# Kernel optimization log

Measured on AMD Instinct MI355X. Metric: run time of the kernel, lower is better.

## Reference

```python
import jax, jax.numpy as jnp
import numpy as np

N, E, F, H, G, U, A = 50000, 800000, 96, 96, 64, 32, 16


def _linear_params(key, fan_in, fan_out):
    # torch nn.Linear default init: U(-1/sqrt(fan_in), 1/sqrt(fan_in))
    s = 1.0 / np.sqrt(fan_in)
    kw, kb = jax.random.split(key)
    W = jax.random.uniform(kw, (fan_in, fan_out), jnp.float32, -s, s)
    b = jax.random.uniform(kb, (fan_out,), jnp.float32, -s, s)
    return W, b


def setup_inputs() -> dict:
    key = jax.random.key(0)
    ks = jax.random.split(key, 12)
    x = jax.random.normal(ks[0], (N, F), jnp.float32)
    edge_index = jax.random.randint(ks[1], (2, E), 0, N, dtype=jnp.int32)
    batch = jnp.sort(jax.random.randint(ks[2], (N,), 0, G, dtype=jnp.int32))
    u = jax.random.normal(ks[3], (G, U), jnp.float32)
    W1, b1 = _linear_params(ks[4], F, H)      # conv1
    W2, b2 = _linear_params(ks[5], H, H)      # conv2
    aW1, ab1 = _linear_params(ks[6], H + U, H)
    aW2, ab2 = _linear_params(ks[7], H, A)
    cW1, cb1 = _linear_params(ks[8], H + U, H)
    cW2, cb2 = _linear_params(ks[9], H, 1)
    return {"x": x, "edge_index": edge_index, "batch": batch, "u": u,
            "W1": W1, "b1": b1, "W2": W2, "b2": b2,
            "aW1": aW1, "ab1": ab1, "aW2": aW2, "ab2": ab2,
            "cW1": cW1, "cb1": cb1, "cW2": cW2, "cb2": cb2}


def reference(x, edge_index, batch, u, W1, b1, W2, b2,
              aW1, ab1, aW2, ab2, cW1, cb1, cW2, cb2):
    n = x.shape[0]
    src, dst = edge_index[0], edge_index[1]
    # GCN symmetric normalization with self-loops (PyG GCNConv defaults)
    deg = jnp.zeros((n,), x.dtype).at[dst].add(1.0) + 1.0  # +1 for self-loop
    dis = jax.lax.rsqrt(deg)                               # deg^{-1/2}
    edge_norm = (dis[src] * dis[dst])[:, None]             # [E,1]
    self_norm = (dis * dis)[:, None]                       # [N,1] = deg^{-1}

    def gcn(h, W, b):
        h = h @ W                                          # linear (bias after agg)
        agg = jax.ops.segment_sum(h[src] * edge_norm, dst, num_segments=n)
        return agg + h * self_norm + b

    h = jax.nn.relu(gcn(x, W1, b1))
    h = jax.nn.relu(gcn(h, W2, b2))

    # global mean pool over graphs
    cnt = jax.ops.segment_sum(jnp.ones((n,), h.dtype), batch, num_segments=G)
    pooled = jax.ops.segment_sum(h, batch, num_segments=G) / jnp.maximum(cnt, 1.0)[:, None]

    comb = jnp.concatenate([pooled, u], axis=1)            # [G, H+U]
    action_logits = jax.nn.relu(comb @ aW1 + ab1) @ aW2 + ab2   # [G, A]
    state_value = jax.nn.relu(comb @ cW1 + cb1) @ cW2 + cb2     # [G, 1]
    return action_logits, state_value
```

## Files before the change

kernel.cpp:

```cpp
#include <hip/hip_runtime.h>
#include <hip/hip_bf16.h>

#define FH 96
#define GU 32
#define GA 16
#define NG 64

typedef __attribute__((ext_vector_type(8))) short bf16x8;
typedef __attribute__((ext_vector_type(8))) unsigned short u16x8;
typedef __attribute__((ext_vector_type(4))) float f32x4;

static __device__ __forceinline__ unsigned short f2bf(float f) {
    unsigned int u = __float_as_uint(f);
    unsigned int r = (u + 0x7fffu + ((u >> 16) & 1u)) >> 16;
    return (unsigned short)r;
}
static __device__ __forceinline__ float bf2f(unsigned short h) {
    return __uint_as_float(((unsigned int)h) << 16);
}

__global__ void zero_k(float4* __restrict__ p, int n4) {
    int i = blockIdx.x * blockDim.x + threadIdx.x;
    if (i < n4) p[i] = make_float4(0.f, 0.f, 0.f, 0.f);
}

__global__ void count_deg_k(const int* __restrict__ dst, int* __restrict__ deg,
                            unsigned short* __restrict__ rank16, int E) {
    int e = blockIdx.x * blockDim.x + threadIdx.x;
    if (e < E) rank16[e] = (unsigned short)atomicAdd(&deg[dst[e]], 1);
}

__global__ __launch_bounds__(256) void partial_k(const int* __restrict__ deg,
                                                 int* __restrict__ blockSums, int n) {
    int base = blockIdx.x * 1024;
    int t = threadIdx.x;
    int s = 0;
#pragma unroll
    for (int j = 0; j < 4; j++) {
        int i = base + t * 4 + j;
        if (i < n) s += deg[i];
    }
    __shared__ int red[4];
    for (int off = 32; off > 0; off >>= 1) s += __shfl_down(s, off, 64);
    if ((t & 63) == 0) red[t >> 6] = s;
    __syncthreads();
    if (t == 0) blockSums[blockIdx.x] = red[0] + red[1] + red[2] + red[3];
}

__global__ __launch_bounds__(256) void scanpart_k(const int* __restrict__ blockSums,
                                                  int* __restrict__ blockOff, int nb) {
    __shared__ int sh[256];
    int t = threadIdx.x;
    sh[t] = (t < nb) ? blockSums[t] : 0;
    __syncthreads();
    for (int off = 1; off < 256; off <<= 1) {
        int v = 0;
        if (t >= off) v = sh[t - off];
        __syncthreads();
        if (t >= off) sh[t] += v;
        __syncthreads();
    }
    if (t < nb) blockOff[t] = (t == 0) ? 0 : sh[t - 1];
}

__global__ __launch_bounds__(256) void emit_k(const int* __restrict__ deg,
                                              const int* __restrict__ blockOff,
                                              int* __restrict__ rowstart,
                                              float* __restrict__ dis, int n) {
    __shared__ int sh[256];
    int base = blockIdx.x * 1024;
    int t = threadIdx.x;
    int d[4];
    int s = 0;
#pragma unroll
    for (int j = 0; j < 4; j++) {
        int i = base + t * 4 + j;
        d[j] = (i < n) ? deg[i] : 0;
        s += d[j];
    }
    sh[t] = s;
    __syncthreads();
    for (int off = 1; off < 256; off <<= 1) {
        int v = 0;
        if (t >= off) v = sh[t - off];
        __syncthreads();
        if (t >= off) sh[t] += v;
        __syncthreads();
    }
    int run = blockOff[blockIdx.x] + ((t == 0) ? 0 : sh[t - 1]);
#pragma unroll
    for (int j = 0; j < 4; j++) {
        int i = base + t * 4 + j;
        if (i < n) {
            rowstart[i] = run;
            dis[i] = rsqrtf((float)d[j] + 1.0f);
        }
        run += d[j];
    }
    if (blockIdx.x == gridDim.x - 1 && t == 255) rowstart[n] = run;
}

__global__ void fill_k(const int* __restrict__ src, const int* __restrict__ dst,
                       const int* __restrict__ rowstart,
                       const unsigned short* __restrict__ rank16,
                       unsigned short* __restrict__ csr, int E) {
    int e = blockIdx.x * blockDim.x + threadIdx.x;
    if (e < E) {
        int pos = rowstart[dst[e]] + (int)rank16[e];
        csr[pos] = (unsigned short)src[e];
    }
}

__global__ __launch_bounds__(256) void convW_k(const float* __restrict__ W1,
                                               const float* __restrict__ W2,
                                               unsigned short* __restrict__ WB1,
                                               unsigned short* __restrict__ WB2) {
    const float* W = (blockIdx.x == 0) ? W1 : W2;
    unsigned short* WB = (blockIdx.x == 0) ? WB1 : WB2;
    for (int idx = threadIdx.x; idx < 2 * 3 * 6 * 64 * 8; idx += 256) {
        int j = idx & 7;
        int lane = (idx >> 3) & 63;
        int frag = idx >> 9;
        int cg = frag % 6;
        int rest = frag / 6;
        int ks = rest % 3;
        int t = rest / 3;
        int k = ks * 32 + (lane >> 4) * 8 + j;
        int n = cg * 16 + (lane & 15);
        float w = W[k * FH + n];
        unsigned short h = f2bf(w);
        WB[idx] = (t == 0) ? h : f2bf(w - bf2f(h));
    }
}

template <int INMODE>
__global__ __launch_bounds__(256, 3) void gemm_mfma_k(
    const float* __restrict__ Xf, const unsigned short* __restrict__ Xb,
    const unsigned short* __restrict__ WB, const float* __restrict__ scale,
    unsigned short* __restrict__ Yb, int nrows) {
    int lane = threadIdx.x & 63;
    int wid  = threadIdx.x >> 6;
    int wr = wid >> 1, wc = wid & 1;
    int row0 = blockIdx.x * 64 + wr * 32;

    bf16x8 b[2][3][3];
#pragma unroll
    for (int t = 0; t < 2; t++)
#pragma unroll
        for (int ks = 0; ks < 3; ks++)
#pragma unroll
            for (int cg = 0; cg < 3; cg++) {
                int frag = (t * 3 + ks) * 6 + wc * 3 + cg;
                b[t][ks][cg] = *(const bf16x8*)(WB + frag * 512 + lane * 8);
            }

    f32x4 acc[2][3];
#pragma unroll
    for (int rg = 0; rg < 2; rg++)
#pragma unroll
        for (int cg = 0; cg < 3; cg++) acc[rg][cg] = (f32x4){0.f, 0.f, 0.f, 0.f};

    int r0 = lane & 15;
    int kcol = (lane >> 4) * 8;
#pragma unroll
    for (int ks = 0; ks < 3; ks++) {
        bf16x8 ah[2], al[2];
#pragma unroll
        for (int rg = 0; rg < 2; rg++) {
            if (INMODE == 1) {
                size_t off = (size_t)(row0 + rg * 16 + r0) * FH + ks * 32 + kcol;
                ah[rg] = *(const bf16x8*)(Xb + off);
            } else {
                int rr = row0 + rg * 16 + r0;
                if (rr >= nrows) rr = nrows - 1;
                const float* xp = Xf + (size_t)rr * FH + ks * 32 + kcol;
                float4 v0 = *(const float4*)xp;
                float4 v1 = *(const float4*)(xp + 4);
                float xv[8] = {v0.x, v0.y, v0.z, v0.w, v1.x, v1.y, v1.z, v1.w};
                bf16x8 hh, ll;
#pragma unroll
                for (int j = 0; j < 8; j++) {
                    unsigned short h = f2bf(xv[j]);
                    hh[j] = (short)h;
                    ll[j] = (short)f2bf(xv[j] - bf2f(h));
                }
                ah[rg] = hh;
                al[rg] = ll;
            }
        }
#pragma unroll
        for (int rg = 0; rg < 2; rg++)
#pragma unroll
            for (int cg = 0; cg < 3; cg++)
                acc[rg][cg] = __builtin_amdgcn_mfma_f32_16x16x32_bf16(
                    ah[rg], b[0][ks][cg], acc[rg][cg], 0, 0, 0);
#pragma unroll
        for (int rg = 0; rg < 2; rg++)
#pragma unroll
            for (int cg = 0; cg < 3; cg++)
                acc[rg][cg] = __builtin_amdgcn_mfma_f32_16x16x32_bf16(
                    ah[rg], b[1][ks][cg], acc[rg][cg], 0, 0, 0);
        if (INMODE == 0) {
#pragma unroll
            for (int rg = 0; rg < 2; rg++)
#pragma unroll
                for (int cg = 0; cg < 3; cg++)
                    acc[rg][cg] = __builtin_amdgcn_mfma_f32_16x16x32_bf16(
                        al[rg], b[0][ks][cg], acc[rg][cg], 0, 0, 0);
        }
    }

#pragma unroll
    for (int rg = 0; rg < 2; rg++) {
#pragma unroll
        for (int r = 0; r < 4; r++) {
            int row = row0 + rg * 16 + (lane >> 4) * 4 + r;
            if (row < nrows) {
                float s = scale[row];
#pragma unroll
                for (int cg = 0; cg < 3; cg++) {
                    int col = wc * 48 + cg * 16 + (lane & 15);
                    Yb[(size_t)row * FH + col] = f2bf(acc[rg][cg][r] * s);
                }
            }
        }
    }
}

__global__ __launch_bounds__(256) void gather12_k(
    const unsigned short* __restrict__ hXb, const float* __restrict__ dis,
    const int* __restrict__ rowstart, const unsigned short* __restrict__ csr,
    const float* __restrict__ bias, unsigned short* __restrict__ outB, int n) {
    int idx = blockIdx.x * blockDim.x + threadIdx.x;
    if (idx >= n * 12) return;
    int node = idx / 12;
    int f8 = (idx - node * 12) * 8;
    int s = rowstart[node];
    int e = rowstart[node + 1];
    u16x8 sv = *(const u16x8*)&hXb[node * FH + f8];
    float a[8];
#pragma unroll
    for (int j = 0; j < 8; j++) a[j] = bf2f((unsigned short)sv[j]);
    int p = s;
    for (; p + 4 <= e; p += 4) {
        int i0 = csr[p], i1 = csr[p + 1], i2 = csr[p + 2], i3 = csr[p + 3];
        u16x8 v0 = *(const u16x8*)&hXb[i0 * FH + f8];
        u16x8 v1 = *(const u16x8*)&hXb[i1 * FH + f8];
        u16x8 v2 = *(const u16x8*)&hXb[i2 * FH + f8];
        u16x8 v3 = *(const u16x8*)&hXb[i3 * FH + f8];
#pragma unroll
        for (int j = 0; j < 8; j++) {
            a[j] += (bf2f((unsigned short)v0[j]) + bf2f((unsigned short)v1[j]))
                  + (bf2f((unsigned short)v2[j]) + bf2f((unsigned short)v3[j]));
        }
    }
    for (; p < e; p++) {
        int i0 = csr[p];
        u16x8 v0 = *(const u16x8*)&hXb[i0 * FH + f8];
#pragma unroll
        for (int j = 0; j < 8; j++) a[j] += bf2f((unsigned short)v0[j]);
    }
    float dn = dis[node];
    float4 bv0 = *(const float4*)&bias[f8];
    float4 bv1 = *(const float4*)&bias[f8 + 4];
    float bb[8] = {bv0.x, bv0.y, bv0.z, bv0.w, bv1.x, bv1.y, bv1.z, bv1.w};
    u16x8 hh;
#pragma unroll
    for (int j = 0; j < 8; j++) hh[j] = f2bf(fmaxf(a[j] * dn + bb[j], 0.0f));
    *(u16x8*)&outB[node * FH + f8] = hh;
}

__global__ __launch_bounds__(128) void pool3_k(const unsigned short* __restrict__ h,
                                               const int* __restrict__ bat,
                                               float* __restrict__ pooled,
                                               float* __restrict__ cnt, int n) {
    const int CH = 32;
    int beg = blockIdx.x * CH;
    if (beg >= n) return;
    int end = min(beg + CH, n);
    int t = threadIdx.x;
    if (t < FH) {
        float acc = 0.f;
        int g = bat[beg];
        for (int node = beg; node < end; ++node) {
            int gg = bat[node];
            if (gg != g) { atomicAdd(&pooled[g * FH + t], acc); acc = 0.f; g = gg; }
            acc += bf2f(h[(size_t)node * FH + t]);
        }
        atomicAdd(&pooled[g * FH + t], acc);
    } else if (t == FH) {
        float c = 0.f;
        int g = bat[beg];
        for (int node = beg; node < end; ++node) {
            int gg = bat[node];
            if (gg != g) { atomicAdd(&cnt[g], c); c = 0.f; g = gg; }
            c += 1.f;
        }
        atomicAdd(&cnt[g], c);
    }
}

__global__ __launch_bounds__(128) void head_k(const float* __restrict__ pooled,
                                              const float* __restrict__ cnt,
                                              const float* __restrict__ u,
                                              const float* __restrict__ aW1, const float* __restrict__ ab1,
                                              const float* __restrict__ aW2, const float* __restrict__ ab2,
                                              const float* __restrict__ cW1, const float* __restrict__ cb1,
                                              const float* __restrict__ cW2, const float* __restrict__ cb2,
                                              float* __restrict__ out, int G) {
    int g = blockIdx.x;
    int t = threadIdx.x;
    __shared__ float comb[FH + GU];
    __shared__ float hidA[FH];
    __shared__ float hidC[FH];
    __shared__ float tmp[FH];
    float c = fmaxf(cnt[g], 1.0f);
    if (t < FH) comb[t] = pooled[g * FH + t] / c;
    else if (t < FH + GU) comb[t] = u[g * GU + (t - FH)];
    __syncthreads();
    if (t < FH) {
        float a = ab1[t], cc = cb1[t];
        for (int k = 0; k < FH + GU; k++) {
            float cv = comb[k];
            a += cv * aW1[k * FH + t];
            cc += cv * cW1[k * FH + t];
        }
        hidA[t] = fmaxf(a, 0.0f);
        hidC[t] = fmaxf(cc, 0.0f);
    }
    __syncthreads();
    if (t < GA) {
        float a = ab2[t];
        for (int j = 0; j < FH; j++) a += hidA[j] * aW2[j * GA + t];
        out[g * GA + t] = a;
    }
    if (t >= 32 && t < 32 + FH) tmp[t - 32] = hidC[t - 32] * cW2[t - 32];
    __syncthreads();
    if (t == 0) {
        float v = cb2[0];
        for (int j = 0; j < FH; j++) v += tmp[j];
        out[G * GA + g] = v;
    }
}

extern "C" void kernel_launch(void* const* d_in, const int* in_sizes, int n_in,
                              void* d_out, int out_size, void* d_ws, size_t ws_size,
                              hipStream_t stream) {
    const float* x   = (const float*)d_in[0];
    const int*   ei  = (const int*)d_in[1];
    const int*   bat = (const int*)d_in[2];
    const float* u   = (const float*)d_in[3];
    const float* W1  = (const float*)d_in[4];
    const float* b1  = (const float*)d_in[5];
    const float* W2  = (const float*)d_in[6];
    const float* b2  = (const float*)d_in[7];
    const float* aW1 = (const float*)d_in[8];
    const float* ab1 = (const float*)d_in[9];
    const float* aW2 = (const float*)d_in[10];
    const float* ab2 = (const float*)d_in[11];
    const float* cW1 = (const float*)d_in[12];
    const float* cb1 = (const float*)d_in[13];
    const float* cW2 = (const float*)d_in[14];
    const float* cb2 = (const float*)d_in[15];
    float* out = (float*)d_out;

    const int N = in_sizes[0] / FH;
    const int E = in_sizes[1] / 2;
    const int G = in_sizes[3] / GU;
    const int NPAD = (N + 63) / 64 * 64;

    const int* src = ei;
    const int* dst = ei + E;

    float* ws = (float*)d_ws;
    size_t o = 0;
    int*   degI     = (int*)(ws + o);   o += NPAD;
    float* pooled   = ws + o;           o += NG * FH;
    float* cnt      = ws + o;           o += 64;
    size_t zero_elems = o;
    float* dis      = ws + o;           o += NPAD;
    int*   rowstart = (int*)(ws + o);   o += NPAD;
    int*   blockSums= (int*)(ws + o);   o += 512;
    int*   blockOff = (int*)(ws + o);   o += 512;
    unsigned short* rank16 = (unsigned short*)(ws + o); o += ((size_t)(E + 1) / 2 + 63) / 64 * 64;
    unsigned short* csr16  = (unsigned short*)(ws + o); o += ((size_t)(E + 1) / 2 + 63) / 64 * 64;
    unsigned short* WB1 = (unsigned short*)(ws + o); o += 9216;
    unsigned short* WB2 = (unsigned short*)(ws + o); o += 9216;
    unsigned short* XhB = (unsigned short*)(ws + o); o += (size_t)NPAD * FH / 2;
    unsigned short* hXb = (unsigned short*)(ws + o); o += (size_t)NPAD * FH / 2;
    (void)ws_size;

    unsigned short* h2b = XhB;

    int gridE = (E + 255) / 256;
    int gridG12 = (N * 12 + 255) / 256;
    int gridMfma = NPAD / 64;
    int nbScan = (N + 1023) / 1024;
    int gridPool = (N + 31) / 32;
    int n4zero = (int)(zero_elems / 4);
    int gridZero = (n4zero + 255) / 256;

    zero_k<<<gridZero, 256, 0, stream>>>((float4*)ws, n4zero);

    count_deg_k<<<gridE, 256, 0, stream>>>(dst, degI, rank16, E);
    partial_k<<<nbScan, 256, 0, stream>>>(degI, blockSums, N);
    scanpart_k<<<1, 256, 0, stream>>>(blockSums, blockOff, nbScan);
    emit_k<<<nbScan, 256, 0, stream>>>(degI, blockOff, rowstart, dis, N);
    fill_k<<<gridE, 256, 0, stream>>>(src, dst, rowstart, rank16, csr16, E);

    convW_k<<<2, 256, 0, stream>>>(W1, W2, WB1, WB2);

    gemm_mfma_k<0><<<gridMfma, 256, 0, stream>>>(x, (const unsigned short*)nullptr,
                                                 WB1, dis, hXb, N);
    gather12_k<<<gridG12, 256, 0, stream>>>(hXb, dis, rowstart, csr16, b1, XhB, N);
    gemm_mfma_k<1><<<gridMfma, 256, 0, stream>>>((const float*)nullptr, XhB,
                                                 WB2, dis, hXb, N);
    gather12_k<<<gridG12, 256, 0, stream>>>(hXb, dis, rowstart, csr16, b2, h2b, N);

    pool3_k<<<gridPool, 128, 0, stream>>>(h2b, bat, pooled, cnt, N);
    head_k<<<G, 128, 0, stream>>>(pooled, cnt, u, aW1, ab1, aW2, ab2,
                                  cW1, cb1, cW2, cb2, out, G);
}
```

Baseline: 182.5 us.

## Fuse CSR preprocessing kernels into one cooperative kernel with grid syncs

Replaces the seven preprocessing launches (zeroing, degree count, partial sums, scan, emit, CSR fill, weight conversion) with a single cooperative kernel of 1024 blocks that separates the phases with grid-wide syncs. The aim is to remove per-launch overhead and the gaps between the small kernels. In exchange it adds five grid barriers and turns the edge loops into grid-stride loops over fewer threads. It also relies on all 1024 blocks being co-resident, and the launch return code is discarded.

```diff
diff --git a/kernel.cpp b/kernel.cpp
--- a/kernel.cpp
+++ b/kernel.cpp
@@ -1,5 +1,6 @@
 #include <hip/hip_runtime.h>
 #include <hip/hip_bf16.h>
+#include <hip/hip_cooperative_groups.h>
 
 #define FH 96
 #define GU 32
@@ -19,117 +20,121 @@
     return __uint_as_float(((unsigned int)h) << 16);
 }
 
-__global__ void zero_k(float4* __restrict__ p, int n4) {
-    int i = blockIdx.x * blockDim.x + threadIdx.x;
-    if (i < n4) p[i] = make_float4(0.f, 0.f, 0.f, 0.f);
-}
-
-__global__ void count_deg_k(const int* __restrict__ dst, int* __restrict__ deg,
-                            unsigned short* __restrict__ rank16, int E) {
-    int e = blockIdx.x * blockDim.x + threadIdx.x;
-    if (e < E) rank16[e] = (unsigned short)atomicAdd(&deg[dst[e]], 1);
-}
-
-__global__ __launch_bounds__(256) void partial_k(const int* __restrict__ deg,
-                                                 int* __restrict__ blockSums, int n) {
-    int base = blockIdx.x * 1024;
-    int t = threadIdx.x;
-    int s = 0;
-#pragma unroll
-    for (int j = 0; j < 4; j++) {
-        int i = base + t * 4 + j;
-        if (i < n) s += deg[i];
-    }
-    __shared__ int red[4];
-    for (int off = 32; off > 0; off >>= 1) s += __shfl_down(s, off, 64);
-    if ((t & 63) == 0) red[t >> 6] = s;
-    __syncthreads();
-    if (t == 0) blockSums[blockIdx.x] = red[0] + red[1] + red[2] + red[3];
-}
-
-__global__ __launch_bounds__(256) void scanpart_k(const int* __restrict__ blockSums,
-                                                  int* __restrict__ blockOff, int nb) {
+__global__ __launch_bounds__(256) void prep_k(
+    const int* __restrict__ src, const int* __restrict__ dst,
+    const float* __restrict__ W1, const float* __restrict__ W2,
+    int* __restrict__ deg, unsigned short* __restrict__ rank16,
+    int* __restrict__ rowstart, float* __restrict__ dis,
+    unsigned short* __restrict__ csr,
+    unsigned short* __restrict__ WB1, unsigned short* __restrict__ WB2,
+    int* __restrict__ blockOff, float* __restrict__ pooled,
+    float* __restrict__ cnt, int N, int E, int nbScan) {
+    cooperative_groups::grid_group gg = cooperative_groups::this_grid();
+    const int gtid = blockIdx.x * blockDim.x + threadIdx.x;
+    const int gsz = gridDim.x * blockDim.x;
     __shared__ int sh[256];
-    int t = threadIdx.x;
-    sh[t] = (t < nb) ? blockSums[t] : 0;
-    __syncthreads();
-    for (int off = 1; off < 256; off <<= 1) {
-        int v = 0;
-        if (t >= off) v = sh[t - off];
-        __syncthreads();
-        if (t >= off) sh[t] += v;
-        __syncthreads();
-    }
-    if (t < nb) blockOff[t] = (t == 0) ? 0 : sh[t - 1];
-}
-
-__global__ __launch_bounds__(256) void emit_k(const int* __restrict__ deg,
-                                              const int* __restrict__ blockOff,
-                                              int* __restrict__ rowstart,
-                                              float* __restrict__ dis, int n) {
-    __shared__ int sh[256];
-    int base = blockIdx.x * 1024;
-    int t = threadIdx.x;
-    int d[4];
-    int s = 0;
-#pragma unroll
-    for (int j = 0; j < 4; j++) {
-        int i = base + t * 4 + j;
-        d[j] = (i < n) ? deg[i] : 0;
-        s += d[j];
-    }
-    sh[t] = s;
-    __syncthreads();
-    for (int off = 1; off < 256; off <<= 1) {
-        int v = 0;
-        if (t >= off) v = sh[t - off];
-        __syncthreads();
-        if (t >= off) sh[t] += v;
-        __syncthreads();
-    }
-    int run = blockOff[blockIdx.x] + ((t == 0) ? 0 : sh[t - 1]);
-#pragma unroll
-    for (int j = 0; j < 4; j++) {
-        int i = base + t * 4 + j;
-        if (i < n) {
-            rowstart[i] = run;
-            dis[i] = rsqrtf((float)d[j] + 1.0f);
-        }
-        run += d[j];
-    }
-    if (blockIdx.x == gridDim.x - 1 && t == 255) rowstart[n] = run;
-}
-
-__global__ void fill_k(const int* __restrict__ src, const int* __restrict__ dst,
-                       const int* __restrict__ rowstart,
-                       const unsigned short* __restrict__ rank16,
-                       unsigned short* __restrict__ csr, int E) {
-    int e = blockIdx.x * blockDim.x + threadIdx.x;
-    if (e < E) {
-        int pos = rowstart[dst[e]] + (int)rank16[e];
-        csr[pos] = (unsigned short)src[e];
-    }
-}
-
-__global__ __launch_bounds__(256) void convW_k(const float* __restrict__ W1,
-                                               const float* __restrict__ W2,
-                                               unsigned short* __restrict__ WB1,
-                                               unsigned short* __restrict__ WB2) {
-    const float* W = (blockIdx.x == 0) ? W1 : W2;
-    unsigned short* WB = (blockIdx.x == 0) ? WB1 : WB2;
-    for (int idx = threadIdx.x; idx < 2 * 3 * 6 * 64 * 8; idx += 256) {
-        int j = idx & 7;
-        int lane = (idx >> 3) & 63;
-        int frag = idx >> 9;
-        int cg = frag % 6;
+
+    for (int i = gtid; i < N; i += gsz) deg[i] = 0;
+    for (int i = gtid; i < NG * FH + NG; i += gsz) {
+        if (i < NG * FH) pooled[i] = 0.f;
+        else cnt[i - NG * FH] = 0.f;
+    }
+    for (int idx = gtid; idx < 2 * 36 * 512; idx += gsz) {
+        int half = idx / (36 * 512);
+        int id2 = idx - half * (36 * 512);
+        const float* W = half ? W2 : W1;
+        unsigned short* WB = half ? WB2 : WB1;
+        int j = id2 & 7;
+        int lane = (id2 >> 3) & 63;
+        int frag = id2 >> 9;
+        int cgi = frag % 6;
         int rest = frag / 6;
         int ks = rest % 3;
         int t = rest / 3;
         int k = ks * 32 + (lane >> 4) * 8 + j;
-        int n = cg * 16 + (lane & 15);
+        int n = cgi * 16 + (lane & 15);
         float w = W[k * FH + n];
         unsigned short h = f2bf(w);
-        WB[idx] = (t == 0) ? h : f2bf(w - bf2f(h));
+        WB[id2] = (t == 0) ? h : f2bf(w - bf2f(h));
+    }
+    gg.sync();
+
+    for (int e = gtid; e < E; e += gsz)
+        rank16[e] = (unsigned short)atomicAdd(&deg[dst[e]], 1);
+    gg.sync();
+
+    if ((int)blockIdx.x < nbScan) {
+        int base = blockIdx.x * 1024;
+        int t = threadIdx.x;
+        int s = 0;
+#pragma unroll
+        for (int j = 0; j < 4; j++) {
+            int i = base + t * 4 + j;
+            if (i < N) s += deg[i];
+        }
+        sh[t] = s;
+        __syncthreads();
+        for (int off = 128; off > 0; off >>= 1) {
+            if (t < off) sh[t] += sh[t + off];
+            __syncthreads();
+        }
+        if (t == 0) blockOff[blockIdx.x] = sh[0];
+    }
+    gg.sync();
+
+    if (blockIdx.x == 0) {
+        int t = threadIdx.x;
+        sh[t] = (t < nbScan) ? blockOff[t] : 0;
+        __syncthreads();
+        for (int off = 1; off < 256; off <<= 1) {
+            int v = 0;
+            if (t >= off) v = sh[t - off];
+            __syncthreads();
+            if (t >= off) sh[t] += v;
+            __syncthreads();
+        }
+        if (t < nbScan) blockOff[t] = (t == 0) ? 0 : sh[t - 1];
+    }
+    gg.sync();
+
+    if ((int)blockIdx.x < nbScan) {
+        int base = blockIdx.x * 1024;
+        int t = threadIdx.x;
+        int d[4];
+        int s = 0;
+#pragma unroll
+        for (int j = 0; j < 4; j++) {
+            int i = base + t * 4 + j;
+            d[j] = (i < N) ? deg[i] : 0;
+            s += d[j];
+        }
+        __syncthreads();
+        sh[t] = s;
+        __syncthreads();
+        for (int off = 1; off < 256; off <<= 1) {
+            int v = 0;
+            if (t >= off) v = sh[t - off];
+            __syncthreads();
+            if (t >= off) sh[t] += v;
+            __syncthreads();
+        }
+        int run = blockOff[blockIdx.x] + ((t == 0) ? 0 : sh[t - 1]);
+#pragma unroll
+        for (int j = 0; j < 4; j++) {
+            int i = base + t * 4 + j;
+            if (i < N) {
+                rowstart[i] = run;
+                dis[i] = rsqrtf((float)d[j] + 1.0f);
+            }
+            run += d[j];
+        }
+        if ((int)blockIdx.x == nbScan - 1 && t == 255) rowstart[N] = run;
+    }
+    gg.sync();
+
+    for (int e = gtid; e < E; e += gsz) {
+        int pos = rowstart[dst[e]] + (int)rank16[e];
+        csr[pos] = (unsigned short)src[e];
     }
 }
 
@@ -377,10 +382,8 @@
     int*   degI     = (int*)(ws + o);   o += NPAD;
     float* pooled   = ws + o;           o += NG * FH;
     float* cnt      = ws + o;           o += 64;
-    size_t zero_elems = o;
     float* dis      = ws + o;           o += NPAD;
     int*   rowstart = (int*)(ws + o);   o += NPAD;
-    int*   blockSums= (int*)(ws + o);   o += 512;
     int*   blockOff = (int*)(ws + o);   o += 512;
     unsigned short* rank16 = (unsigned short*)(ws + o); o += ((size_t)(E + 1) / 2 + 63) / 64 * 64;
     unsigned short* csr16  = (unsigned short*)(ws + o); o += ((size_t)(E + 1) / 2 + 63) / 64 * 64;
@@ -392,23 +395,22 @@
 
     unsigned short* h2b = XhB;
 
-    int gridE = (E + 255) / 256;
     int gridG12 = (N * 12 + 255) / 256;
     int gridMfma = NPAD / 64;
     int nbScan = (N + 1023) / 1024;
     int gridPool = (N + 31) / 32;
-    int n4zero = (int)(zero_elems / 4);
-    int gridZero = (n4zero + 255) / 256;
-
-    zero_k<<<gridZero, 256, 0, stream>>>((float4*)ws, n4zero);
-
-    count_deg_k<<<gridE, 256, 0, stream>>>(dst, degI, rank16, E);
-    partial_k<<<nbScan, 256, 0, stream>>>(degI, blockSums, N);
-    scanpart_k<<<1, 256, 0, stream>>>(blockSums, blockOff, nbScan);
-    emit_k<<<nbScan, 256, 0, stream>>>(degI, blockOff, rowstart, dis, N);
-    fill_k<<<gridE, 256, 0, stream>>>(src, dst, rowstart, rank16, csr16, E);
-
-    convW_k<<<2, 256, 0, stream>>>(W1, W2, WB1, WB2);
+
+    {
+        int Nl = N, El = E, nbl = nbScan;
+        void* args[] = {
+            (void*)&src, (void*)&dst, (void*)&W1, (void*)&W2,
+            (void*)&degI, (void*)&rank16, (void*)&rowstart, (void*)&dis,
+            (void*)&csr16, (void*)&WB1, (void*)&WB2, (void*)&blockOff,
+            (void*)&pooled, (void*)&cnt, (void*)&Nl, (void*)&El, (void*)&nbl
+        };
+        (void)hipLaunchCooperativeKernel((const void*)prep_k, dim3(1024),
+                                         dim3(256), args, 0, stream);
+    }
 
     gemm_mfma_k<0><<<gridMfma, 256, 0, stream>>>(x, (const unsigned short*)nullptr,
                                                  WB1, dis, hXb, N);
```

New measurement: 654.0 us. +258.4%, slower.
